# Kernel tuning notes

Hardware: AMD Instinct MI355X
Metric: run time of the kernel (lower is better)

Reference implementation:

```python
import jax, jax.numpy as jnp
import numpy as np

B, N, M, DQ, DK, DV, H = 8, 1024, 1024, 512, 512, 512, 8
DH = DV // H           # per-head dim (dim_split)
DFF = 4 * DV           # FFN hidden dim
EPS = 1e-5


def _layernorm(x, g, b):
    mu = jnp.mean(x, axis=-1, keepdims=True)
    var = jnp.mean(jnp.square(x - mu), axis=-1, keepdims=True)
    return (x - mu) * jax.lax.rsqrt(var + EPS) * g + b


def setup_inputs() -> dict:
    key = jax.random.key(0)
    ks = jax.random.split(key, 20)
    s = 0.02
    return {
        "Q": jax.random.normal(ks[0], (B, N, DQ), jnp.float32),
        "K": jax.random.normal(ks[1], (B, M, DK), jnp.float32),
        "Wq": jax.random.normal(ks[2], (DV, DQ), jnp.float32) * s,
        "bq": jnp.zeros((DV,), jnp.float32),
        "Wk": jax.random.normal(ks[3], (DV, DK), jnp.float32) * s,
        "bk": jnp.zeros((DV,), jnp.float32),
        "Wv": jax.random.normal(ks[4], (DV, DK), jnp.float32) * s,
        "bv": jnp.zeros((DV,), jnp.float32),
        "W1": jax.random.normal(ks[5], (DFF, DV), jnp.float32) * s,
        "b1": jnp.zeros((DFF,), jnp.float32),
        "W2": jax.random.normal(ks[6], (DFF, DFF), jnp.float32) * s,
        "b2": jnp.zeros((DFF,), jnp.float32),
        "W3": jax.random.normal(ks[7], (DV, DFF), jnp.float32) * s,
        "b3": jnp.zeros((DV,), jnp.float32),
        "g0": jnp.ones((DV,), jnp.float32),
        "beta0": jnp.zeros((DV,), jnp.float32),
        "g1": jnp.ones((DV,), jnp.float32),
        "beta1": jnp.zeros((DV,), jnp.float32),
    }


def reference(Q, K, Wq, bq, Wk, bk, Wv, bv, W1, b1, W2, b2, W3, b3, g0, beta0, g1, beta1):
    # projections (torch Linear: x @ W.T + b)
    Qp = Q @ Wq.T + bq            # [B, N, DV]
    Kp = K @ Wk.T + bk            # [B, M, DV]
    Vp = K @ Wv.T + bv            # [B, M, DV]

    # split heads: [B, S, DV] -> [B, S, H, DH]
    Qh = Qp.reshape(B, N, H, DH)
    Kh = Kp.reshape(B, M, H, DH)
    Vh = Vp.reshape(B, M, H, DH)

    # scaled dot-product attention (scale = sqrt(head_dim))
    A = jnp.einsum("bnhd,bmhd->bhnm", Qh, Kh) / jnp.sqrt(jnp.float32(DH))
    A = jax.nn.softmax(A, axis=-1)
    O = jnp.einsum("bhnm,bmhd->bnhd", A, Vh).reshape(B, N, DV)

    # residual with projected Q, then LN
    O = _layernorm(O + Qp, g0, beta0)

    # FFN: Linear->ReLU->Linear->ReLU->Linear (num_hidden_layers=2)
    h = jax.nn.relu(O @ W1.T + b1)
    h = jax.nn.relu(h @ W2.T + b2)
    Off = h @ W3.T + b3

    return _layernorm(O + Off, g1, beta1)
```

## Files before the change

kernel.cpp:

```cpp
#include <hip/hip_runtime.h>


typedef __bf16 bf16_t;
typedef __bf16 bf16x8 __attribute__((ext_vector_type(8)));
typedef __bf16 bf16x4 __attribute__((ext_vector_type(4)));
typedef __bf16 bf16x2 __attribute__((ext_vector_type(2)));
typedef float  f32x4  __attribute__((ext_vector_type(4)));
typedef float  f32x16 __attribute__((ext_vector_type(16)));
typedef int    i32x4_t __attribute__((ext_vector_type(4)));
typedef int    i32x8_t __attribute__((ext_vector_type(8)));

__device__ __forceinline__ f32x4 mfma16(bf16x8 a, bf16x8 b, f32x4 c) {
  return __builtin_amdgcn_mfma_f32_16x16x32_bf16(a, b, c, 0, 0, 0);
}

__device__ __forceinline__ void gload_lds16(const void* g, void* l) {
  __builtin_amdgcn_global_load_lds((const __attribute__((address_space(1))) void*)g,
                                   (__attribute__((address_space(3))) void*)l,
                                   16, 0, 0);
}

__device__ __forceinline__ unsigned char to_fp8(float v) {
  return (unsigned char)(__builtin_amdgcn_cvt_pk_fp8_f32(v, v, 0, false) & 0xff);
}

__global__ __launch_bounds__(256) void cast_all(
    const float* __restrict__ Q, const float* __restrict__ K,
    const float* __restrict__ Wq, const float* __restrict__ Wk,
    const float* __restrict__ Wv, const float* __restrict__ W1,
    const float* __restrict__ W2, const float* __restrict__ W3,
    bf16_t* Qb, bf16_t* Kb, bf16_t* Wqb, bf16_t* Wkb, bf16_t* Wvb,
    bf16_t* W1b, unsigned char* W2q, bf16_t* W3b)
{
  long i = ((long)blockIdx.x * 256 + threadIdx.x) * 4;
  if (i >= 10223616L && i < 14417920L) {
    long o = i - 10223616L;
    float4 v = *(const float4*)(W2 + o);
    unsigned int lo = __builtin_amdgcn_cvt_pk_fp8_f32(v.x, v.y, 0, false);
    unsigned int hi = __builtin_amdgcn_cvt_pk_fp8_f32(v.z, v.w, 0, false);
    *(unsigned int*)(W2q + o) = (lo & 0xffffu) | (hi << 16);
    return;
  }
  const float* s; bf16_t* d; long o;
  if      (i <  4194304L) { s = Q;  d = Qb;  o = i;             }
  else if (i <  8388608L) { s = K;  d = Kb;  o = i - 4194304L;  }
  else if (i <  8650752L) { s = Wq; d = Wqb; o = i - 8388608L;  }
  else if (i <  8912896L) { s = Wk; d = Wkb; o = i - 8650752L;  }
  else if (i <  9175040L) { s = Wv; d = Wvb; o = i - 8912896L;  }
  else if (i < 10223616L) { s = W1; d = W1b; o = i - 9175040L;  }
  else                    { s = W3; d = W3b; o = i - 14417920L; }
  float4 v = *(const float4*)(s + o);
  bf16x4 w;
  w[0] = (bf16_t)v.x; w[1] = (bf16_t)v.y; w[2] = (bf16_t)v.z; w[3] = (bf16_t)v.w;
  *(bf16x4*)(d + o) = w;
}

template <int BM, bool RELU, bool VTEPI>
__device__ __forceinline__ void gemm_core(
    const bf16_t* __restrict__ A, const bf16_t* __restrict__ W,
    const float* __restrict__ bias, float* __restrict__ Cf,
    bf16_t* __restrict__ Cb, unsigned char* __restrict__ C8,
    bf16_t* __restrict__ VTout,
    float bscale, int N, int K, int lda, int ldb, int bx, int by)
{
  constexpr int WM = (BM == 128) ? 2 : 1;
  constexpr int WN = 4 / WM;
  constexpr int FI = 4;
  constexpr int FJ = 128 / (WN * 16);
  constexpr int CN = 128 / WN;
  constexpr int AISS = BM / 32;
  constexpr int SM_AB = (BM + 128) * 64 * 2;
  constexpr int SM_TS = 128 * 132 * 2;
  constexpr int SMEM = (VTEPI && SM_TS > SM_AB) ? SM_TS : SM_AB;

  __shared__ __align__(16) char smem[SMEM];
  bf16_t* As = (bf16_t*)smem;
  bf16_t* Bs = (bf16_t*)(smem + BM * 64 * 2);

  const int tid  = threadIdx.x;
  const int wave = tid >> 6, lane = tid & 63;
  const int lq   = lane & 15, quad = lane >> 4;
  const int wm   = (WM == 2) ? (wave & 1) : 0;
  const int wn   = (WM == 2) ? (wave >> 1) : wave;
  const long row0 = (long)bx * BM;
  const long col0 = (long)by * 128;

  const int sr = tid >> 3;
  const int cg = (tid & 7) ^ (sr & 7);
  const bf16_t* ag = A + (row0 + sr) * (long)lda + cg * 8;
  const bf16_t* bg = W + (col0 + sr) * (long)ldb + cg * 8;
  char* asD = (char*)As + wave * 1024;
  char* bsD = (char*)Bs + wave * 1024;

  const int off0 = (quad ^ (lq & 7)) * 8;
  const bf16_t* aR0 = As + (wm * 64 + lq) * 64 + off0;
  const bf16_t* aR1 = As + (wm * 64 + lq) * 64 + (off0 ^ 32);
  const bf16_t* bR0 = Bs + (wn * CN + lq) * 64 + off0;
  const bf16_t* bR1 = Bs + (wn * CN + lq) * 64 + (off0 ^ 32);

  f32x4 acc[FI][FJ];
#pragma unroll
  for (int i = 0; i < FI; i++)
#pragma unroll
    for (int j = 0; j < FJ; j++) acc[i][j] = (f32x4){0.f, 0.f, 0.f, 0.f};

  const long arows32 = 32L * lda;
  const long brows32 = 32L * ldb;
  for (int k0 = 0; k0 < K; k0 += 64) {
    __syncthreads();
#pragma unroll
    for (int is = 0; is < AISS; is++)
      gload_lds16(ag + is * arows32 + k0, asD + is * 4096);
#pragma unroll
    for (int is = 0; is < 4; is++)
      gload_lds16(bg + is * brows32 + k0, bsD + is * 4096);
    __syncthreads();
    bf16x8 af[FI], bw[FJ];
#pragma unroll
    for (int i = 0; i < FI; i++) af[i] = *(const bf16x8*)(aR0 + i * 1024);
#pragma unroll
    for (int j = 0; j < FJ; j++) bw[j] = *(const bf16x8*)(bR0 + j * 1024);
#pragma unroll
    for (int i = 0; i < FI; i++)
#pragma unroll
      for (int j = 0; j < FJ; j++)
        acc[i][j] = mfma16(af[i], bw[j], acc[i][j]);
#pragma unroll
    for (int i = 0; i < FI; i++) af[i] = *(const bf16x8*)(aR1 + i * 1024);
#pragma unroll
    for (int j = 0; j < FJ; j++) bw[j] = *(const bf16x8*)(bR1 + j * 1024);
#pragma unroll
    for (int i = 0; i < FI; i++)
#pragma unroll
      for (int j = 0; j < FJ; j++)
        acc[i][j] = mfma16(af[i], bw[j], acc[i][j]);
  }

  float bc[FJ];
#pragma unroll
  for (int j = 0; j < FJ; j++)
    bc[j] = bias ? bias[col0 + wn * CN + j * 16 + lq] : 0.f;

  if (VTEPI && VTout) {
    bf16_t* Ts = (bf16_t*)smem;
    __syncthreads();
#pragma unroll
    for (int i = 0; i < FI; i++)
#pragma unroll
      for (int j = 0; j < FJ; j++) {
        bf16x4 pv;
#pragma unroll
        for (int r = 0; r < 4; r++) pv[r] = (bf16_t)(acc[i][j][r] + bc[j]);
        *(bf16x4*)(Ts + (wn * CN + j * 16 + lq) * 132 + wm * 64 + i * 16 + quad * 4) = pv;
      }
    __syncthreads();
    const int b  = bx >> 3;
    const int mb = (bx & 7) * 128;
    const int h0 = by * 2;
    const int dd = tid >> 4;
    const int mc = (tid & 15) * 8;
#pragma unroll
    for (int p = 0; p < 8; p++) {
      const int d = dd + p * 16;
      bf16x8 v = *(const bf16x8*)(Ts + d * 132 + mc);
      *(bf16x8*)(VTout + ((long)(b * 8 + h0 + (d >> 6))) * 65536
                 + (d & 63) * 1024 + mb + mc) = v;
    }
    return;
  }

  const long rb = row0 + wm * 64 + quad * 4;
  const long cb = col0 + wn * CN + lq;
#pragma unroll
  for (int i = 0; i < FI; i++)
#pragma unroll
    for (int j = 0; j < FJ; j++)
#pragma unroll
      for (int r = 0; r < 4; r++) {
        float v = acc[i][j][r] + bc[j];
        if (RELU) v = fmaxf(v, 0.f);
        long idx = (rb + i * 16 + r) * (long)N + cb + j * 16;
        if (Cf) Cf[idx] = v;
        if (Cb) Cb[idx] = (bf16_t)(v * bscale);
        if (C8) C8[idx] = to_fp8(v);
      }
}

template <int BM, bool RELU>
__global__ __launch_bounds__(256) void gemm_bt(
    const bf16_t* __restrict__ A, const bf16_t* __restrict__ W,
    const float* __restrict__ bias, float* __restrict__ Cf,
    bf16_t* __restrict__ Cb, unsigned char* __restrict__ C8,
    float bscale, int N, int K)
{
  gemm_core<BM, RELU, false>(A, W, bias, Cf, Cb, C8, nullptr, bscale,
                             N, K, K, K, blockIdx.x, blockIdx.y);
}

__global__ __launch_bounds__(256) void ffn3_splitk(
    const bf16_t* __restrict__ H2, const bf16_t* __restrict__ W3b,
    bf16_t* __restrict__ Off01)
{
  const int z = blockIdx.z;
  gemm_core<128, false, false>(H2 + z * 1024, W3b + z * 1024, nullptr,
                               nullptr, Off01 + (long)z * 4194304, nullptr,
                               nullptr, 1.0f, 512, 1024, 2048, 2048,
                               blockIdx.x, blockIdx.y);
}

__global__ __launch_bounds__(256) void proj3(
    const bf16_t* __restrict__ Qb, const bf16_t* __restrict__ Kb,
    const bf16_t* __restrict__ Wqb, const bf16_t* __restrict__ Wkb,
    const bf16_t* __restrict__ Wvb,
    const float* __restrict__ bq, const float* __restrict__ bk,
    const float* __restrict__ bv,
    bf16_t* Qpb, bf16_t* Kpb, bf16_t* VT)
{
  const int z = blockIdx.z;
  const bf16_t* A  = (z == 0) ? Qb : Kb;
  const bf16_t* Wt = (z == 0) ? Wqb : ((z == 1) ? Wkb : Wvb);
  const float* bias = (z == 0) ? bq : ((z == 1) ? bk : bv);
  bf16_t* Cb = (z == 0) ? Qpb : ((z == 1) ? Kpb : nullptr);
  bf16_t* VTout = (z == 2) ? VT : nullptr;
  const float sc = (z == 1) ? 0.125f : 1.0f;
  gemm_core<128, false, true>(A, Wt, bias, nullptr, Cb, nullptr, VTout, sc,
                              512, 512, 512, 512, blockIdx.x, blockIdx.y);
}

__global__ __launch_bounds__(256) void ffn2_fp8(
    const unsigned char* __restrict__ H1, const unsigned char* __restrict__ W2,
    const float* __restrict__ bias, bf16_t* __restrict__ C)
{
  __shared__ unsigned char As[16384];
  __shared__ unsigned char Bs[16384];
  const int tid = threadIdx.x;
  const int wave = tid >> 6, lane = tid & 63;
  const int wm = wave & 1, wn = wave >> 1;
  const int m = lane & 31, h = lane >> 5;
  const long row0 = (long)blockIdx.x * 128;
  const long col0 = (long)blockIdx.y * 128;

  const int sr = tid >> 3;
  const int cg = (tid & 7) ^ (sr & 7);
  const unsigned char* ag = H1 + (row0 + sr) * 2048 + cg * 16;
  const unsigned char* bg = W2 + (col0 + sr) * 2048 + cg * 16;
  char* asD = (char*)As + wave * 1024;
  char* bsD = (char*)Bs + wave * 1024;

  const int ar0 = wm * 64 + m, ar1 = ar0 + 32;
  const int br0 = wn * 64 + m, br1 = br0 + 32;

  f32x16 acc[2][2];
#pragma unroll
  for (int mi = 0; mi < 2; mi++)
#pragma unroll
    for (int nj = 0; nj < 2; nj++)
#pragma unroll
      for (int r = 0; r < 16; r++) acc[mi][nj][r] = 0.f;

  for (int k0 = 0; k0 < 2048; k0 += 128) {
    __syncthreads();
#pragma unroll
    for (int is = 0; is < 4; is++)
      gload_lds16(ag + is * 65536 + k0, asD + is * 4096);
#pragma unroll
    for (int is = 0; is < 4; is++)
      gload_lds16(bg + is * 65536 + k0, bsD + is * 4096);
    __syncthreads();
#pragma unroll
    for (int ks = 0; ks < 2; ks++) {
      const int c0 = ks * 4 + h * 2;
      i32x8_t a[2], b[2];
#pragma unroll
      for (int mi = 0; mi < 2; mi++) {
        const int r = mi ? ar1 : ar0;
        i32x4_t lo = *(const i32x4_t*)(As + r * 128 + ((c0    ) ^ (r & 7)) * 16);
        i32x4_t hi = *(const i32x4_t*)(As + r * 128 + ((c0 + 1) ^ (r & 7)) * 16);
        a[mi][0] = lo[0]; a[mi][1] = lo[1]; a[mi][2] = lo[2]; a[mi][3] = lo[3];
        a[mi][4] = hi[0]; a[mi][5] = hi[1]; a[mi][6] = hi[2]; a[mi][7] = hi[3];
      }
#pragma unroll
      for (int nj = 0; nj < 2; nj++) {
        const int r = nj ? br1 : br0;
        i32x4_t lo = *(const i32x4_t*)(Bs + r * 128 + ((c0    ) ^ (r & 7)) * 16);
        i32x4_t hi = *(const i32x4_t*)(Bs + r * 128 + ((c0 + 1) ^ (r & 7)) * 16);
        b[nj][0] = lo[0]; b[nj][1] = lo[1]; b[nj][2] = lo[2]; b[nj][3] = lo[3];
        b[nj][4] = hi[0]; b[nj][5] = hi[1]; b[nj][6] = hi[2]; b[nj][7] = hi[3];
      }
#pragma unroll
      for (int mi = 0; mi < 2; mi++)
#pragma unroll
        for (int nj = 0; nj < 2; nj++)
          acc[mi][nj] = __builtin_amdgcn_mfma_scale_f32_32x32x64_f8f6f4(
              a[mi], b[nj], acc[mi][nj], 0, 0,
              0, 0x7f7f7f7f, 0, 0x7f7f7f7f);
    }
  }

  float bc[2];
  bc[0] = bias[col0 + wn * 64 + m];
  bc[1] = bias[col0 + wn * 64 + 32 + m];
#pragma unroll
  for (int mi = 0; mi < 2; mi++)
#pragma unroll
    for (int nj = 0; nj < 2; nj++)
#pragma unroll
      for (int reg = 0; reg < 16; reg++) {
        const int rl = (reg & 3) + 8 * (reg >> 2) + 4 * h;
        float v = fmaxf(acc[mi][nj][reg] + bc[nj], 0.f);
        C[(row0 + wm * 64 + mi * 32 + rl) * 2048 + col0 + wn * 64 + nj * 32 + m]
            = (bf16_t)v;
      }
}

__global__ __launch_bounds__(256) void attn(
    const bf16_t* __restrict__ Qp, const bf16_t* __restrict__ Kp,
    const bf16_t* __restrict__ VT, bf16_t* __restrict__ O)
{
  const int qb = blockIdx.x, h = blockIdx.y, b = blockIdx.z;
  const int tid = threadIdx.x;
  const int wave = tid >> 6, lane = tid & 63;
  const int lq = lane & 15, quad = lane >> 4;

  __shared__ bf16_t Ks[8192];
  __shared__ bf16_t VTs[8192];
  __shared__ bf16_t Ps[4][16 * 72];

  const long bh = (long)b * 1024;
  const int qrow = qb * 64 + wave * 16 + lq;

  const bf16_t* qptr = Qp + (bh + qrow) * 512 + h * 64 + quad * 8;
  const bf16x8 qf0 = *(const bf16x8*)qptr;
  const bf16x8 qf1 = *(const bf16x8*)(qptr + 32);

  f32x4 oacc[4];
#pragma unroll
  for (int t = 0; t < 4; t++) oacc[t] = (f32x4){0.f, 0.f, 0.f, 0.f};
  float l_i = 0.f;

  const int sr = tid >> 3;
  const int cg = (tid & 7) ^ (sr & 7);
  char* ksDst = (char*)Ks + wave * 1024;
  char* vtDst = (char*)VTs + wave * 1024;
  const bf16_t* kg  = Kp + bh * 512 + h * 64;
  const bf16_t* vtg = VT + ((long)b * 8 + h) * 65536;
  const int off0 = (quad ^ (lq & 7)) * 8;

  for (int m0 = 0; m0 < 1024; m0 += 128) {
    __syncthreads();
#pragma unroll
    for (int s = 0; s < 2; s++) {
      gload_lds16(kg + (long)(m0 + s * 64 + sr) * 512 + cg * 8,      ksDst + s * 8192);
      gload_lds16(kg + (long)(m0 + s * 64 + sr + 32) * 512 + cg * 8, ksDst + s * 8192 + 4096);
      gload_lds16(vtg + (long)sr * 1024 + m0 + s * 64 + cg * 8,        vtDst + s * 8192);
      gload_lds16(vtg + (long)(sr + 32) * 1024 + m0 + s * 64 + cg * 8, vtDst + s * 8192 + 4096);
    }
    __syncthreads();

    f32x4 st[8];
#pragma unroll
    for (int t = 0; t < 8; t++) {
      const bf16_t* kb = Ks + (t >> 2) * 4096 + ((t & 3) * 16 + lq) * 64;
      bf16x8 ka0 = *(const bf16x8*)(kb + off0);
      bf16x8 ka1 = *(const bf16x8*)(kb + (off0 ^ 32));
      f32x4 s = (f32x4){0.f, 0.f, 0.f, 0.f};
      s = mfma16(ka0, qf0, s);
      s = mfma16(ka1, qf1, s);
      st[t] = s;
    }
    float lsum = 0.f;
#pragma unroll
    for (int t = 0; t < 8; t++)
#pragma unroll
      for (int r = 0; r < 4; r++) {
        float p = __expf(st[t][r]);
        st[t][r] = p;
        lsum += p;
      }
    lsum += __shfl_xor(lsum, 16, 64);
    lsum += __shfl_xor(lsum, 32, 64);
    l_i += lsum;

    bf16_t* pw = &Ps[wave][0];
#pragma unroll
    for (int hh = 0; hh < 2; hh++) {
#pragma unroll
      for (int t = 0; t < 4; t++) {
        bf16x4 pv;
#pragma unroll
        for (int r = 0; r < 4; r++) pv[r] = (bf16_t)st[hh * 4 + t][r];
        *(bf16x4*)(pw + lq * 72 + t * 16 + quad * 4) = pv;
      }
#pragma unroll
      for (int ks = 0; ks < 2; ks++) {
        bf16x8 pb = *(const bf16x8*)(pw + lq * 72 + ks * 32 + quad * 8);
#pragma unroll
        for (int dt = 0; dt < 4; dt++) {
          const bf16_t* vb = VTs + hh * 4096 + (dt * 16 + lq) * 64;
          bf16x8 va = *(const bf16x8*)(vb + (ks ? (off0 ^ 32) : off0));
          oacc[dt] = mfma16(va, pb, oacc[dt]);
        }
      }
    }
  }

  const float inv = 1.f / l_i;
  bf16_t* op = O + (bh + qrow) * 512 + h * 64 + quad * 4;
#pragma unroll
  for (int dt = 0; dt < 4; dt++) {
    bf16x4 v;
#pragma unroll
    for (int r = 0; r < 4; r++) v[r] = (bf16_t)(oacc[dt][r] * inv);
    *(bf16x4*)(op + dt * 16) = v;
  }
}

__device__ __forceinline__ float2 ld2(const float* p, long row, int tid) {
  return ((const float2*)(p + row * 512))[tid];
}
__device__ __forceinline__ float2 ld2(const bf16_t* p, long row, int tid) {
  bf16x2 v = *(const bf16x2*)(p + row * 512 + tid * 2);
  return make_float2((float)v[0], (float)v[1]);
}

__device__ __forceinline__ void ln_finish(
    float x0, float x1, const float* g, const float* be, int tid,
    int wave, int lane, float* of, bf16_t* ob, long row)
{
  float s = x0 + x1, ss = x0 * x0 + x1 * x1;
#pragma unroll
  for (int off = 1; off < 64; off <<= 1) {
    s  += __shfl_xor(s,  off, 64);
    ss += __shfl_xor(ss, off, 64);
  }
  __shared__ float sm[8];
  if (lane == 0) { sm[wave] = s; sm[4 + wave] = ss; }
  __syncthreads();
  s  = sm[0] + sm[1] + sm[2] + sm[3];
  ss = sm[4] + sm[5] + sm[6] + sm[7];
  const float mu = s * (1.f / 512.f);
  const float var = ss * (1.f / 512.f) - mu * mu;
  const float rs = rsqrtf(var + 1e-5f);
  const float2 gg = ((const float2*)g)[tid];
  const float2 bb = ((const float2*)be)[tid];
  const float o0 = (x0 - mu) * rs * gg.x + bb.x;
  const float o1 = (x1 - mu) * rs * gg.y + bb.y;
  if (of) ((float2*)(of + row * 512))[tid] = make_float2(o0, o1);
  if (ob) {
    bf16x2 t; t[0] = (bf16_t)o0; t[1] = (bf16_t)o1;
    *(bf16x2*)(ob + row * 512 + tid * 2) = t;
  }
}

__global__ __launch_bounds__(256) void ln_res(
    const bf16_t* __restrict__ A, const bf16_t* __restrict__ Bv,
    const float* __restrict__ g, const float* __restrict__ be,
    bf16_t* __restrict__ ob)
{
  const int row = blockIdx.x, tid = threadIdx.x;
  const float2 va = ld2(A,  (long)row, tid);
  const float2 vb = ld2(Bv, (long)row, tid);
  ln_finish(va.x + vb.x, va.y + vb.y, g, be, tid, tid >> 6, tid & 63,
            nullptr, ob, row);
}

__global__ __launch_bounds__(256) void ln_res3(
    const bf16_t* __restrict__ X, const bf16_t* __restrict__ O0,
    const bf16_t* __restrict__ O1, const float* __restrict__ bias,
    const float* __restrict__ g, const float* __restrict__ be,
    float* __restrict__ of)
{
  const int row = blockIdx.x, tid = threadIdx.x;
  const float2 vx = ld2(X,  (long)row, tid);
  const float2 v0 = ld2(O0, (long)row, tid);
  const float2 v1 = ld2(O1, (long)row, tid);
  const float2 vb = ((const float2*)bias)[tid];
  ln_finish(vx.x + v0.x + v1.x + vb.x, vx.y + v0.y + v1.y + vb.y,
            g, be, tid, tid >> 6, tid & 63, of, nullptr, row);
}

extern "C" void kernel_launch(void* const* d_in, const int* in_sizes, int n_in,
                              void* d_out, int out_size, void* d_ws, size_t ws_size,
                              hipStream_t stream)
{
  const float* Q   = (const float*)d_in[0];
  const float* K   = (const float*)d_in[1];
  const float* Wq  = (const float*)d_in[2];
  const float* bq  = (const float*)d_in[3];
  const float* Wk  = (const float*)d_in[4];
  const float* bk  = (const float*)d_in[5];
  const float* Wv  = (const float*)d_in[6];
  const float* bv  = (const float*)d_in[7];
  const float* W1  = (const float*)d_in[8];
  const float* b1  = (const float*)d_in[9];
  const float* W2  = (const float*)d_in[10];
  const float* b2  = (const float*)d_in[11];
  const float* W3  = (const float*)d_in[12];
  const float* b3  = (const float*)d_in[13];
  const float* g0  = (const float*)d_in[14];
  const float* be0 = (const float*)d_in[15];
  const float* g1  = (const float*)d_in[16];
  const float* be1 = (const float*)d_in[17];

  char* ws = (char*)d_ws;
  bf16_t* Wqb = (bf16_t*)(ws + 0);
  bf16_t* Wkb = (bf16_t*)(ws + 524288);
  bf16_t* Wvb = (bf16_t*)(ws + 1048576);
  bf16_t* W1b = (bf16_t*)(ws + 1572864);
  bf16_t* W3b = (bf16_t*)(ws + 3670016);
  unsigned char* W2q = (unsigned char*)(ws + 5767168);
  bf16_t* Qb  = (bf16_t*)(ws + 14155776);
  bf16_t* Kb  = (bf16_t*)(ws + 22544384);
  bf16_t* Qpb = (bf16_t*)(ws + 30932992);
  bf16_t* Kpb = (bf16_t*)(ws + 39321600);
  bf16_t* VT  = (bf16_t*)(ws + 47710208);
  bf16_t* Of  = (bf16_t*)(ws + 14155776);
  bf16_t* Xb  = (bf16_t*)(ws + 22544384);
  bf16_t* H2  = (bf16_t*)(ws + 30932992);
  unsigned char* H1q = (unsigned char*)(ws + 64487424);
  bf16_t* Off0 = (bf16_t*)(ws + 64487424);
  bf16_t* Off1 = (bf16_t*)(ws + 72876032);
  float*  out = (float*)d_out;

  cast_all<<<15104, 256, 0, stream>>>(Q, K, Wq, Wk, Wv, W1, W2, W3,
                                      Qb, Kb, Wqb, Wkb, Wvb, W1b, W2q, W3b);
  proj3<<<dim3(64, 4, 3), 256, 0, stream>>>(Qb, Kb, Wqb, Wkb, Wvb, bq, bk, bv,
                                            Qpb, Kpb, VT);
  attn<<<dim3(16, 8, 8), 256, 0, stream>>>(Qpb, Kpb, VT, Of);
  ln_res<<<8192, 256, 0, stream>>>(Of, Qpb, g0, be0, Xb);
  gemm_bt<128, true ><<<dim3(64, 16), 256, 0, stream>>>(Xb, W1b, b1, nullptr, nullptr, H1q, 1.0f, 2048, 512);
  ffn2_fp8<<<dim3(64, 16), 256, 0, stream>>>(H1q, W2q, b2, H2);
  ffn3_splitk<<<dim3(64, 4, 2), 256, 0, stream>>>(H2, W3b, Off0);
  ln_res3<<<8192, 256, 0, stream>>>(Xb, Off0, Off1, b3, g1, be1, out);
}
```

Before: 295.7 us.

## Double-buffer K/V tiles in attention and remap blocks for XCD locality

The attention kernel now double-buffers the K and V^T LDS tiles. It issues the global-to-LDS loads for the next 128-key tile before computing on the current one, using explicit vmcnt waits and barriers in place of the two full syncthreads per iteration. The grid is flattened to one dimension with a swizzled mapping, so blocks of the same (batch, head) land on the same XCD and share K/V in L2. LDS use doubles to about 73KB per block, which may reduce how many blocks fit on a CU.

```diff
diff --git a/kernel.cpp b/kernel.cpp
--- a/kernel.cpp
+++ b/kernel.cpp
@@ -317,13 +317,18 @@
     const bf16_t* __restrict__ Qp, const bf16_t* __restrict__ Kp,
     const bf16_t* __restrict__ VT, bf16_t* __restrict__ O)
 {
-  const int qb = blockIdx.x, h = blockIdx.y, b = blockIdx.z;
+  const int d0 = blockIdx.x;
+  const int j  = d0 >> 3;
+  const int g  = (d0 & 7) * 8 + (j >> 4);
+  const int qb = j & 15;
+  const int h  = g & 7, b = g >> 3;
+
   const int tid = threadIdx.x;
   const int wave = tid >> 6, lane = tid & 63;
   const int lq = lane & 15, quad = lane >> 4;
 
-  __shared__ bf16_t Ks[8192];
-  __shared__ bf16_t VTs[8192];
+  __shared__ bf16_t Ks[2][8192];
+  __shared__ bf16_t VTs[2][8192];
   __shared__ bf16_t Ps[4][16 * 72];
 
   const long bh = (long)b * 1024;
@@ -340,14 +345,13 @@
 
   const int sr = tid >> 3;
   const int cg = (tid & 7) ^ (sr & 7);
-  char* ksDst = (char*)Ks + wave * 1024;
-  char* vtDst = (char*)VTs + wave * 1024;
   const bf16_t* kg  = Kp + bh * 512 + h * 64;
   const bf16_t* vtg = VT + ((long)b * 8 + h) * 65536;
   const int off0 = (quad ^ (lq & 7)) * 8;
 
-  for (int m0 = 0; m0 < 1024; m0 += 128) {
-    __syncthreads();
+  auto stage = [&](int m0, int bi) {
+    char* ksDst = (char*)(Ks[bi]) + wave * 1024;
+    char* vtDst = (char*)(VTs[bi]) + wave * 1024;
 #pragma unroll
     for (int s = 0; s < 2; s++) {
       gload_lds16(kg + (long)(m0 + s * 64 + sr) * 512 + cg * 8,      ksDst + s * 8192);
@@ -355,26 +359,42 @@
       gload_lds16(vtg + (long)sr * 1024 + m0 + s * 64 + cg * 8,        vtDst + s * 8192);
       gload_lds16(vtg + (long)(sr + 32) * 1024 + m0 + s * 64 + cg * 8, vtDst + s * 8192 + 4096);
     }
-    __syncthreads();
+  };
+
+  stage(0, 0);
+
+  for (int t = 0; t < 8; ++t) {
+    const int cur = t & 1;
+    if (t < 7) {
+      stage((t + 1) * 128, cur ^ 1);
+      asm volatile("s_waitcnt vmcnt(8)" ::: "memory");
+    } else {
+      asm volatile("s_waitcnt vmcnt(0)" ::: "memory");
+    }
+    __builtin_amdgcn_s_barrier();
+    __builtin_amdgcn_sched_barrier(0);
+
+    const bf16_t* Kc = Ks[cur];
+    const bf16_t* Vc = VTs[cur];
 
     f32x4 st[8];
 #pragma unroll
-    for (int t = 0; t < 8; t++) {
-      const bf16_t* kb = Ks + (t >> 2) * 4096 + ((t & 3) * 16 + lq) * 64;
+    for (int tt = 0; tt < 8; tt++) {
+      const bf16_t* kb = Kc + (tt >> 2) * 4096 + ((tt & 3) * 16 + lq) * 64;
       bf16x8 ka0 = *(const bf16x8*)(kb + off0);
       bf16x8 ka1 = *(const bf16x8*)(kb + (off0 ^ 32));
       f32x4 s = (f32x4){0.f, 0.f, 0.f, 0.f};
       s = mfma16(ka0, qf0, s);
       s = mfma16(ka1, qf1, s);
-      st[t] = s;
+      st[tt] = s;
     }
     float lsum = 0.f;
 #pragma unroll
-    for (int t = 0; t < 8; t++)
+    for (int tt = 0; tt < 8; tt++)
 #pragma unroll
       for (int r = 0; r < 4; r++) {
-        float p = __expf(st[t][r]);
-        st[t][r] = p;
+        float p = __expf(st[tt][r]);
+        st[tt][r] = p;
         lsum += p;
       }
     lsum += __shfl_xor(lsum, 16, 64);
@@ -385,23 +405,26 @@
 #pragma unroll
     for (int hh = 0; hh < 2; hh++) {
 #pragma unroll
-      for (int t = 0; t < 4; t++) {
+      for (int tt = 0; tt < 4; tt++) {
         bf16x4 pv;
 #pragma unroll
-        for (int r = 0; r < 4; r++) pv[r] = (bf16_t)st[hh * 4 + t][r];
-        *(bf16x4*)(pw + lq * 72 + t * 16 + quad * 4) = pv;
+        for (int r = 0; r < 4; r++) pv[r] = (bf16_t)st[hh * 4 + tt][r];
+        *(bf16x4*)(pw + lq * 72 + tt * 16 + quad * 4) = pv;
       }
 #pragma unroll
       for (int ks = 0; ks < 2; ks++) {
         bf16x8 pb = *(const bf16x8*)(pw + lq * 72 + ks * 32 + quad * 8);
 #pragma unroll
         for (int dt = 0; dt < 4; dt++) {
-          const bf16_t* vb = VTs + hh * 4096 + (dt * 16 + lq) * 64;
+          const bf16_t* vb = Vc + hh * 4096 + (dt * 16 + lq) * 64;
           bf16x8 va = *(const bf16x8*)(vb + (ks ? (off0 ^ 32) : off0));
           oacc[dt] = mfma16(va, pb, oacc[dt]);
         }
       }
     }
+
+    __builtin_amdgcn_sched_barrier(0);
+    __builtin_amdgcn_s_barrier();
   }
 
   const float inv = 1.f / l_i;
@@ -526,7 +549,7 @@
                                       Qb, Kb, Wqb, Wkb, Wvb, W1b, W2q, W3b);
   proj3<<<dim3(64, 4, 3), 256, 0, stream>>>(Qb, Kb, Wqb, Wkb, Wvb, bq, bk, bv,
                                             Qpb, Kpb, VT);
-  attn<<<dim3(16, 8, 8), 256, 0, stream>>>(Qpb, Kpb, VT, Of);
+  attn<<<dim3(1024, 1, 1), 256, 0, stream>>>(Qpb, Kpb, VT, Of);
   ln_res<<<8192, 256, 0, stream>>>(Of, Qpb, g0, be0, Xb);
   gemm_bt<128, true ><<<dim3(64, 16), 256, 0, stream>>>(Xb, W1b, b1, nullptr, nullptr, H1q, 1.0f, 2048, 512);
   ffn2_fp8<<<dim3(64, 16), 256, 0, stream>>>(H1q, W2q, b2, H2);
```

Measured after the change: 285.9 us. 1.03x faster.
